# Kernel tuning notes

Measured on AMD Instinct MI355X. Metric: run time of the kernel, lower is better.

## Reference

```python
import jax, jax.numpy as jnp
import numpy as np

D_MODEL = 1024
N_HEAD = 16
HEAD_DIM = D_MODEL // N_HEAD
BATCH = 2
SEQ = 2048


def setup_inputs() -> dict:
    key = jax.random.key(0)
    ks = jax.random.split(key, 5)
    std = np.sqrt(2.0 / (D_MODEL + D_MODEL)).astype(np.float32)
    return {
        "in_features": jax.random.normal(ks[0], (BATCH, SEQ, D_MODEL), dtype=jnp.float32),
        "Wq": jax.random.normal(ks[1], (D_MODEL, D_MODEL), dtype=jnp.float32) * std,
        "Wk": jax.random.normal(ks[2], (D_MODEL, D_MODEL), dtype=jnp.float32) * std,
        "Wv": jax.random.normal(ks[3], (D_MODEL, D_MODEL), dtype=jnp.float32) * std,
        "Wo": jax.random.normal(ks[4], (D_MODEL, D_MODEL), dtype=jnp.float32) * std,
    }


def reference(in_features, Wq, Wk, Wv, Wo):
    B, S, _ = in_features.shape
    # projections: x @ W (custom Linear stores weight as [in, out], no bias)
    q = (in_features @ Wq).reshape(B, S, N_HEAD, HEAD_DIM).transpose(0, 2, 1, 3)  # [B,H,S,Dh]
    k = (in_features @ Wk).reshape(B, S, N_HEAD, HEAD_DIM).transpose(0, 2, 1, 3)
    v = (in_features @ Wv).reshape(B, S, N_HEAD, HEAD_DIM).transpose(0, 2, 1, 3)
    scale = HEAD_DIM ** (-0.5)
    scores = jnp.einsum("bhqd,bhkd->bhqk", q, k) * scale  # [B,H,S,S]
    causal = jnp.tril(jnp.ones((S, S), dtype=bool))
    scores = jnp.where(causal, scores, -jnp.inf)
    attn = jax.nn.softmax(scores, axis=-1)
    ctx = jnp.einsum("bhqk,bhkd->bhqd", attn, v)  # [B,H,S,Dh]
    ctx = ctx.transpose(0, 2, 1, 3).reshape(B, S, D_MODEL)
    return ctx @ Wo
```

## Files before the change

kernel.cpp:

```cpp
#include <hip/hip_runtime.h>
#include <hip/hip_bf16.h>

#define DM 1024
#define NH 16
#define HD 64
#define B_ 2
#define S_ 2048
#define M_ (B_*S_)

typedef __attribute__((ext_vector_type(8))) short bf16x8;
typedef __attribute__((ext_vector_type(4))) float f32x4;
typedef __attribute__((ext_vector_type(4))) unsigned uint32x4;
typedef __attribute__((ext_vector_type(2))) unsigned uint32x2;

__device__ __forceinline__ float bf2f(ushort u) {
  union { unsigned u32; float f; } c; c.u32 = ((unsigned)u) << 16; return c.f;
}
__device__ __forceinline__ ushort f2bf(float f) {
  union { float f; unsigned u32; } c; c.f = f;
  unsigned u = c.u32;
  unsigned r = (u + 0x7fffu + ((u >> 16) & 1u)) >> 16;
  return (ushort)r;
}
__device__ __forceinline__ unsigned fbits(float f) {
  union { float f; unsigned u; } c; c.f = f; return c.u;
}

__device__ __forceinline__ void async16(const ushort* g, ushort* l) {
  __builtin_amdgcn_global_load_lds((const __attribute__((address_space(1))) void*)g,
                                   (__attribute__((address_space(3))) void*)l, 16, 0, 0);
}

__device__ __forceinline__ void pswap32(unsigned& a, unsigned& b) {
  uint32x2 r = __builtin_amdgcn_permlane32_swap(a, b, false, false);
  a = r[0]; b = r[1];
}
__device__ __forceinline__ void pswap16(unsigned& a, unsigned& b) {
  uint32x2 r = __builtin_amdgcn_permlane16_swap(a, b, false, false);
  a = r[0]; b = r[1];
}

__global__ void cvt_prep(const float* __restrict__ x, const float* __restrict__ W0,
                         const float* __restrict__ W1, const float* __restrict__ W2,
                         const float* __restrict__ W3, ushort* __restrict__ wt,
                         ushort* __restrict__ xb) {
  __shared__ float tile[64][65];
  int z = blockIdx.z;
  int tx = threadIdx.x, ty = threadIdx.y;
  if (z == 4) {
    int tid = ty * 64 + tx;
    size_t base4 = ((size_t)blockIdx.y * 16 + blockIdx.x) * 4096;
    const float4* xv = (const float4*)x;
    ushort4* ov = (ushort4*)xb;
    #pragma unroll
    for (int k = 0; k < 16; ++k) {
      float4 v = xv[base4 + k * 256 + tid];
      ushort4 o;
      o.x = f2bf(v.x); o.y = f2bf(v.y); o.z = f2bf(v.z); o.w = f2bf(v.w);
      ov[base4 + k * 256 + tid] = o;
    }
    return;
  }
  const float* W = (z == 0) ? W0 : (z == 1) ? W1 : (z == 2) ? W2 : W3;
  ushort* Wt = wt + (size_t)z * (DM * DM);
  int c0 = blockIdx.x * 64, r0 = blockIdx.y * 64;
  #pragma unroll
  for (int i = ty; i < 64; i += 4) tile[i][tx] = W[(size_t)(r0 + i) * DM + c0 + tx];
  __syncthreads();
  #pragma unroll
  for (int i = ty; i < 64; i += 4) Wt[(size_t)(c0 + i) * DM + r0 + tx] = f2bf(tile[tx][i]);
}

template <int MODE, int BN>
__device__ __forceinline__ void gemm_body(const ushort* __restrict__ A,
                                          const ushort* __restrict__ Bt,
                                          ushort* __restrict__ Cb,
                                          float* __restrict__ Cf,
                                          ushort* As, ushort* Bs, ushort* Ts) {
  const int K = DM;
  constexpr int CN = BN / 32;
  int m0 = blockIdx.y * 128;
  int n0 = blockIdx.x * BN;
  int t = threadIdx.x;
  int lane = t & 63, wave = t >> 6;
  int wm = (wave >> 1) * 64, wn = (wave & 1) * (BN / 2);
  int lrow = lane & 15, quad = lane >> 4;

  int Ra = wave * 32;
  int Rb = wave * (BN / 4);
  int srow = lane >> 2, scol = (lane & 3) * 8;

  f32x4 acc[4][CN];
  #pragma unroll
  for (int r = 0; r < 4; ++r)
    #pragma unroll
    for (int c = 0; c < CN; ++c) acc[r][c] = (f32x4){0.f, 0.f, 0.f, 0.f};

  for (int k0 = 0; k0 < K; k0 += 32) {
    const ushort* ga = A + (size_t)(m0 + Ra + srow) * K + k0 + scol;
    const ushort* gb = Bt + (size_t)(n0 + Rb + srow) * K + k0 + scol;
    async16(ga,          As + Ra * 32);
    async16(ga + 16 * K, As + (Ra + 16) * 32);
    async16(gb,          Bs + Rb * 32);
    if (BN == 128) async16(gb + 16 * K, Bs + (Rb + 16) * 32);
    __syncthreads();

    bf16x8 af[4], bfr[CN];
    #pragma unroll
    for (int r = 0; r < 4; ++r)
      af[r] = *(const bf16x8*)(As + (wm + r * 16 + lrow) * 32 + quad * 8);
    #pragma unroll
    for (int c = 0; c < CN; ++c)
      bfr[c] = *(const bf16x8*)(Bs + (wn + c * 16 + lrow) * 32 + quad * 8);
    #pragma unroll
    for (int r = 0; r < 4; ++r)
      #pragma unroll
      for (int c = 0; c < CN; ++c)
        acc[r][c] = __builtin_amdgcn_mfma_f32_16x16x32_bf16(af[r], bfr[c], acc[r][c], 0, 0, 0);
    __syncthreads();
  }

  if constexpr (MODE == 2) {
    int bb = m0 >> 11;
    int s0base = m0 & 2047;
    #pragma unroll
    for (int H = 0; H < 2; ++H) {
      __syncthreads();
      if ((wave >> 1) == H) {
        #pragma unroll
        for (int r = 0; r < 4; ++r)
          #pragma unroll
          for (int c = 0; c < 4; ++c) {
            uint2 pk;
            pk.x = (unsigned)f2bf(acc[r][c][0]) | ((unsigned)f2bf(acc[r][c][1]) << 16);
            pk.y = (unsigned)f2bf(acc[r][c][2]) | ((unsigned)f2bf(acc[r][c][3]) << 16);
            *(uint2*)(Ts + (wn + c * 16 + lrow) * 72 + r * 16 + quad * 4) = pk;
          }
      }
      __syncthreads();
      #pragma unroll
      for (int i = 0; i < 4; ++i) {
        int id = t + i * 256;
        int nn = id >> 3, col = (id & 7) * 8;
        uint4 v = *(const uint4*)(Ts + nn * 72 + col);
        int h2 = (n0 >> 6) + (nn >> 6), d2 = nn & 63;
        size_t dst = (((size_t)(bb * NH + h2)) * HD + d2) * (size_t)S_ + s0base + H * 64 + col;
        *(uint4*)(Cb + dst) = v;
      }
    }
  } else {
    #pragma unroll
    for (int r = 0; r < 4; ++r) {
      #pragma unroll
      for (int c = 0; c < CN; ++c) {
        #pragma unroll
        for (int e = 0; e < 4; ++e) {
          int m = m0 + wm + r * 16 + quad * 4 + e;
          int n = n0 + wn + c * 16 + lrow;
          if (MODE == 0) {
            Cf[(size_t)m * DM + n] = acc[r][c][e];
          } else {
            int b = m >> 11, s = m & 2047, h = n >> 6, d = n & 63;
            Cb[(((size_t)(b * NH + h)) * S_ + s) * HD + d] = f2bf(acc[r][c][e]);
          }
        }
      }
    }
  }
}

__global__ __launch_bounds__(256, 3) void gemm_qkv(const ushort* __restrict__ A,
                                                   const ushort* __restrict__ wt,
                                                   ushort* __restrict__ qkv) {
  __shared__ __align__(16) ushort smem[9216];
  ushort* As = smem;
  ushort* Bs = smem + 4096;
  ushort* Ts = smem;
  int z = blockIdx.z;
  if (z < 2)
    gemm_body<1, 128>(A, wt + (size_t)z * (DM * DM), qkv + (size_t)z * ((size_t)M_ * DM),
                      nullptr, As, Bs, Ts);
  else
    gemm_body<2, 128>(A, wt + (size_t)2 * (DM * DM), qkv + (size_t)2 * ((size_t)M_ * DM),
                      nullptr, As, Bs, Ts);
}

__global__ __launch_bounds__(256, 3) void gemm_out(const ushort* __restrict__ A,
                                                   const ushort* __restrict__ wt,
                                                   float* __restrict__ C) {
  __shared__ __align__(16) ushort As[128 * 32];
  __shared__ __align__(16) ushort Bs[64 * 32];
  gemm_body<0, 64>(A, wt, nullptr, C, As, Bs, nullptr);
}

#define EXPC 0.18033688011f

struct AttnState {
  f32x4 o[4];
  float l;
};

template <bool MASKED>
__device__ __forceinline__ void attn_tile_compute(
    int q0, int kt, bf16x8 qf0, bf16x8 qf1,
    const bf16x8 kf0[4], const bf16x8 kf1[4],
    const bf16x8 vf0[4], const bf16x8 vf1[4],
    AttnState& st, int lrow, int quad) {
  f32x4 s[4];
  #pragma unroll
  for (int c = 0; c < 4; ++c) {
    f32x4 z = (f32x4){0.f, 0.f, 0.f, 0.f};
    z = __builtin_amdgcn_mfma_f32_16x16x32_bf16(kf0[c], qf0, z, 0, 0, 0);
    z = __builtin_amdgcn_mfma_f32_16x16x32_bf16(kf1[c], qf1, z, 0, 0, 0);
    s[c] = z;
  }
  int q = q0 + lrow;
  unsigned w0[4], w1[4];
  #pragma unroll
  for (int c = 0; c < 4; ++c) {
    float pv[4];
    #pragma unroll
    for (int e = 0; e < 4; ++e) {
      float v = __builtin_amdgcn_exp2f(s[c][e] * EXPC);
      if (MASKED) {
        int key = kt + c * 16 + quad * 4 + e;
        v = (key <= q) ? v : 0.f;
      }
      pv[e] = v;
      st.l += v;
    }
    w0[c] = __builtin_amdgcn_perm(fbits(pv[1]), fbits(pv[0]), 0x07060302u);
    w1[c] = __builtin_amdgcn_perm(fbits(pv[3]), fbits(pv[2]), 0x07060302u);
  }

  unsigned a0 = w0[0], b0 = w0[1]; pswap32(a0, b0); pswap16(a0, b0);
  unsigned a1 = w1[0], b1 = w1[1]; pswap32(a1, b1); pswap16(a1, b1);
  unsigned c0 = w0[2], d0 = w0[3]; pswap32(c0, d0); pswap16(c0, d0);
  unsigned c1 = w1[2], d1 = w1[3]; pswap32(c1, d1); pswap16(c1, d1);
  union { uint32x4 u; bf16x8 b; } P0, P1;
  P0.u = (uint32x4){a0, a1, b0, b1};
  P1.u = (uint32x4){c0, c1, d0, d1};

  #pragma unroll
  for (int dt = 0; dt < 4; ++dt) {
    st.o[dt] = __builtin_amdgcn_mfma_f32_16x16x32_bf16(P0.b, vf0[dt], st.o[dt], 0, 0, 0);
    st.o[dt] = __builtin_amdgcn_mfma_f32_16x16x32_bf16(P1.b, vf1[dt], st.o[dt], 0, 0, 0);
  }
}

__global__ __launch_bounds__(256, 2) void attn_mfma(const ushort* __restrict__ Q,
                                                    const ushort* __restrict__ Kmat,
                                                    const ushort* __restrict__ Vt,
                                                    ushort* __restrict__ ctx) {
  __shared__ __align__(16) ushort Ks[2][64 * 72];
  __shared__ __align__(16) ushort Vs[2][64 * 72];
  int t = threadIdx.x;
  int lane = t & 63, wave = t >> 6;
  int lrow = lane & 15, quad = lane >> 4;
  int n = blockIdx.x;
  int c = n & 255, g = n >> 8;
  int bh = c & 31;
  int j = (c >> 5) & 7;
  int qt = (g == 0) ? j : (g == 1) ? (15 - j) : (g == 2) ? (16 + j) : (31 - j);
  const ushort* Kb = Kmat + (size_t)bh * S_ * HD;
  const ushort* Vb = Vt + (size_t)bh * HD * S_;
  int b = bh >> 4, h = bh & 15;

  int r0 = t >> 3, s0 = (t & 7) * 8;
  int r1 = (t + 256) >> 3, s1 = s0;

  int q0 = qt * 64 + wave * 16;
  const ushort* Qp = Q + ((size_t)bh * S_ + q0) * HD;
  bf16x8 qf0 = *(const bf16x8*)(Qp + (size_t)lrow * HD + quad * 8);
  bf16x8 qf1 = *(const bf16x8*)(Qp + (size_t)lrow * HD + 32 + quad * 8);

  AttnState st;
  #pragma unroll
  for (int i = 0; i < 4; ++i) st.o[i] = (f32x4){0.f, 0.f, 0.f, 0.f};
  st.l = 0.f;

  int kend = qt * 64;

  {
    uint4 ka = *(const uint4*)(Kb + (size_t)r0 * HD + s0);
    uint4 kb2 = *(const uint4*)(Kb + (size_t)r1 * HD + s1);
    uint4 va = *(const uint4*)(Vb + (size_t)r0 * S_ + s0);
    uint4 vb2 = *(const uint4*)(Vb + (size_t)r1 * S_ + s1);
    *(uint4*)(Ks[0] + r0 * 72 + s0) = ka;
    *(uint4*)(Ks[0] + r1 * 72 + s1) = kb2;
    *(uint4*)(Vs[0] + r0 * 72 + s0) = va;
    *(uint4*)(Vs[0] + r1 * 72 + s1) = vb2;
  }
  __syncthreads();

  for (int kt = 0; kt <= kend; kt += 64) {
    int cur = (kt >> 6) & 1, nxt = cur ^ 1;
    bool has_next = (kt < kend);

    uint4 ka, kb2, va, vb2;
    if (has_next) {
      int ktn = kt + 64;
      ka  = *(const uint4*)(Kb + (size_t)(ktn + r0) * HD + s0);
      kb2 = *(const uint4*)(Kb + (size_t)(ktn + r1) * HD + s1);
      va  = *(const uint4*)(Vb + (size_t)r0 * S_ + ktn + s0);
      vb2 = *(const uint4*)(Vb + (size_t)r1 * S_ + ktn + s1);
    }

    bf16x8 kf0[4], kf1[4], vf0[4], vf1[4];
    #pragma unroll
    for (int c2 = 0; c2 < 4; ++c2) {
      const ushort* kr = Ks[cur] + (c2 * 16 + lrow) * 72;
      kf0[c2] = *(const bf16x8*)(kr + quad * 8);
      kf1[c2] = *(const bf16x8*)(kr + 32 + quad * 8);
      const ushort* vr = Vs[cur] + (c2 * 16 + lrow) * 72;
      vf0[c2] = *(const bf16x8*)(vr + quad * 8);
      vf1[c2] = *(const bf16x8*)(vr + 32 + quad * 8);
    }

    if (kt < kend)
      attn_tile_compute<false>(q0, kt, qf0, qf1, kf0, kf1, vf0, vf1, st, lrow, quad);
    else
      attn_tile_compute<true>(q0, kt, qf0, qf1, kf0, kf1, vf0, vf1, st, lrow, quad);

    if (has_next) {
      *(uint4*)(Ks[nxt] + r0 * 72 + s0) = ka;
      *(uint4*)(Ks[nxt] + r1 * 72 + s1) = kb2;
      *(uint4*)(Vs[nxt] + r0 * 72 + s0) = va;
      *(uint4*)(Vs[nxt] + r1 * 72 + s1) = vb2;
    }
    __syncthreads();
  }

  {
    float l = st.l;
    l += __shfl_xor(l, 16);
    l += __shfl_xor(l, 32);
    float rl = 1.0f / l;
    #pragma unroll
    for (int e = 0; e < 4; ++e) {
      float rinv = __shfl(rl, quad * 4 + e);
      int q = q0 + quad * 4 + e;
      #pragma unroll
      for (int dt = 0; dt < 4; ++dt)
        ctx[((size_t)b * S_ + q) * DM + h * HD + dt * 16 + lrow] = f2bf(st.o[dt][e] * rinv);
    }
  }
}

extern "C" void kernel_launch(void* const* d_in, const int* in_sizes, int n_in,
                              void* d_out, int out_size, void* d_ws, size_t ws_size,
                              hipStream_t stream) {
  const float* x  = (const float*)d_in[0];
  const float* Wq = (const float*)d_in[1];
  const float* Wk = (const float*)d_in[2];
  const float* Wv = (const float*)d_in[3];
  const float* Wo = (const float*)d_in[4];
  float* out = (float*)d_out;
  ushort* ws = (ushort*)d_ws;

  ushort* xb  = ws;
  ushort* wt  = xb + (size_t)M_ * DM;
  ushort* qkv = wt + (size_t)4 * DM * DM;
  ushort* ctx = qkv + (size_t)3 * M_ * DM;

  cvt_prep<<<dim3(16, 16, 5), dim3(64, 4), 0, stream>>>(x, Wq, Wk, Wv, Wo, wt, xb);
  gemm_qkv<<<dim3(DM / 128, M_ / 128, 3), 256, 0, stream>>>(xb, wt, qkv);
  attn_mfma<<<dim3(32 * B_ * NH), 256, 0, stream>>>(qkv, qkv + (size_t)M_ * DM,
                                                    qkv + (size_t)2 * M_ * DM, ctx);
  gemm_out<<<dim3(DM / 64, M_ / 128), 256, 0, stream>>>(ctx, wt + (size_t)3 * DM * DM, out);
}
```

Baseline: 177.0 us.

## Process two adjacent query tiles per attention block to reuse K/V tiles

Each attention block now handles 128 query rows, as two 64-row halves, instead of 64. Each K/V tile loaded into shared memory is applied to both halves, with the lower half stopping one tile earlier at its own diagonal. The grid shrinks from 1024 to 512 blocks, and the query-tile ordering is simplified to pair short and long blocks. This halves K/V global loads and LDS staging per query, but doubles per-thread register state, which may reduce occupancy. The smaller grid also risks leaving compute units underused on a large GPU.

```diff
diff --git a/kernel.cpp b/kernel.cpp
--- a/kernel.cpp
+++ b/kernel.cpp
@@ -261,7 +261,7 @@
   int c = n & 255, g = n >> 8;
   int bh = c & 31;
   int j = (c >> 5) & 7;
-  int qt = (g == 0) ? j : (g == 1) ? (15 - j) : (g == 2) ? (16 + j) : (31 - j);
+  int qt = g ? (15 - j) : j;
   const ushort* Kb = Kmat + (size_t)bh * S_ * HD;
   const ushort* Vb = Vt + (size_t)bh * HD * S_;
   int b = bh >> 4, h = bh & 15;
@@ -269,17 +269,25 @@
   int r0 = t >> 3, s0 = (t & 7) * 8;
   int r1 = (t + 256) >> 3, s1 = s0;
 
-  int q0 = qt * 64 + wave * 16;
-  const ushort* Qp = Q + ((size_t)bh * S_ + q0) * HD;
-  bf16x8 qf0 = *(const bf16x8*)(Qp + (size_t)lrow * HD + quad * 8);
-  bf16x8 qf1 = *(const bf16x8*)(Qp + (size_t)lrow * HD + 32 + quad * 8);
-
-  AttnState st;
-  #pragma unroll
-  for (int i = 0; i < 4; ++i) st.o[i] = (f32x4){0.f, 0.f, 0.f, 0.f};
-  st.l = 0.f;
-
-  int kend = qt * 64;
+  int q0L = qt * 128 + wave * 16;
+  int q0U = q0L + 64;
+  const ushort* QpL = Q + ((size_t)bh * S_ + q0L) * HD;
+  const ushort* QpU = Q + ((size_t)bh * S_ + q0U) * HD;
+  bf16x8 qL0 = *(const bf16x8*)(QpL + (size_t)lrow * HD + quad * 8);
+  bf16x8 qL1 = *(const bf16x8*)(QpL + (size_t)lrow * HD + 32 + quad * 8);
+  bf16x8 qU0 = *(const bf16x8*)(QpU + (size_t)lrow * HD + quad * 8);
+  bf16x8 qU1 = *(const bf16x8*)(QpU + (size_t)lrow * HD + 32 + quad * 8);
+
+  AttnState stL, stU;
+  #pragma unroll
+  for (int i = 0; i < 4; ++i) {
+    stL.o[i] = (f32x4){0.f, 0.f, 0.f, 0.f};
+    stU.o[i] = (f32x4){0.f, 0.f, 0.f, 0.f};
+  }
+  stL.l = 0.f; stU.l = 0.f;
+
+  int kend = (2 * qt + 1) * 64;
+  int kendL = kend - 64;
 
   {
     uint4 ka = *(const uint4*)(Kb + (size_t)r0 * HD + s0);
@@ -318,9 +326,13 @@
     }
 
     if (kt < kend)
-      attn_tile_compute<false>(q0, kt, qf0, qf1, kf0, kf1, vf0, vf1, st, lrow, quad);
+      attn_tile_compute<false>(q0U, kt, qU0, qU1, kf0, kf1, vf0, vf1, stU, lrow, quad);
     else
-      attn_tile_compute<true>(q0, kt, qf0, qf1, kf0, kf1, vf0, vf1, st, lrow, quad);
+      attn_tile_compute<true>(q0U, kt, qU0, qU1, kf0, kf1, vf0, vf1, stU, lrow, quad);
+    if (kt < kendL)
+      attn_tile_compute<false>(q0L, kt, qL0, qL1, kf0, kf1, vf0, vf1, stL, lrow, quad);
+    else if (kt == kendL)
+      attn_tile_compute<true>(q0L, kt, qL0, qL1, kf0, kf1, vf0, vf1, stL, lrow, quad);
 
     if (has_next) {
       *(uint4*)(Ks[nxt] + r0 * 72 + s0) = ka;
@@ -331,7 +343,10 @@
     __syncthreads();
   }
 
-  {
+  #pragma unroll
+  for (int half = 0; half < 2; ++half) {
+    AttnState& st = half ? stU : stL;
+    int q0 = half ? q0U : q0L;
     float l = st.l;
     l += __shfl_xor(l, 16);
     l += __shfl_xor(l, 32);
@@ -365,7 +380,7 @@
 
   cvt_prep<<<dim3(16, 16, 5), dim3(64, 4), 0, stream>>>(x, Wq, Wk, Wv, Wo, wt, xb);
   gemm_qkv<<<dim3(DM / 128, M_ / 128, 3), 256, 0, stream>>>(xb, wt, qkv);
-  attn_mfma<<<dim3(32 * B_ * NH), 256, 0, stream>>>(qkv, qkv + (size_t)M_ * DM,
+  attn_mfma<<<dim3(16 * B_ * NH), 256, 0, stream>>>(qkv, qkv + (size_t)M_ * DM,
                                                     qkv + (size_t)2 * M_ * DM, ctx);
   gemm_out<<<dim3(DM / 64, M_ / 128), 256, 0, stream>>>(ctx, wt + (size_t)3 * DM * DM, out);
 }
```

New measurement: 182.3 us. 3.0% more time.

## Load K/V fragments directly from global memory, dropping LDS staging and barriers

Applied to the files above, without the earlier changes.

The attention kernel no longer stages K and V tiles through double-buffered shared memory. Each wave now loads its MFMA fragments straight from global memory, which removes the LDS writes, the LDS reads and the per-iteration __syncthreads. The cost is that each of the four waves fetches the same K/V data separately, so the kernel leans on L1/L2 for reuse. The software prefetch of the next tile is also gone, so global load latency is no longer overlapped with compute.

```diff
diff --git a/kernel.cpp b/kernel.cpp
--- a/kernel.cpp
+++ b/kernel.cpp
@@ -252,8 +252,6 @@
                                                     const ushort* __restrict__ Kmat,
                                                     const ushort* __restrict__ Vt,
                                                     ushort* __restrict__ ctx) {
-  __shared__ __align__(16) ushort Ks[2][64 * 72];
-  __shared__ __align__(16) ushort Vs[2][64 * 72];
   int t = threadIdx.x;
   int lane = t & 63, wave = t >> 6;
   int lrow = lane & 15, quad = lane >> 4;
@@ -266,9 +264,6 @@
   const ushort* Vb = Vt + (size_t)bh * HD * S_;
   int b = bh >> 4, h = bh & 15;
 
-  int r0 = t >> 3, s0 = (t & 7) * 8;
-  int r1 = (t + 256) >> 3, s1 = s0;
-
   int q0 = qt * 64 + wave * 16;
   const ushort* Qp = Q + ((size_t)bh * S_ + q0) * HD;
   bf16x8 qf0 = *(const bf16x8*)(Qp + (size_t)lrow * HD + quad * 8);
@@ -281,54 +276,26 @@
 
   int kend = qt * 64;
 
-  {
-    uint4 ka = *(const uint4*)(Kb + (size_t)r0 * HD + s0);
-    uint4 kb2 = *(const uint4*)(Kb + (size_t)r1 * HD + s1);
-    uint4 va = *(const uint4*)(Vb + (size_t)r0 * S_ + s0);
-    uint4 vb2 = *(const uint4*)(Vb + (size_t)r1 * S_ + s1);
-    *(uint4*)(Ks[0] + r0 * 72 + s0) = ka;
-    *(uint4*)(Ks[0] + r1 * 72 + s1) = kb2;
-    *(uint4*)(Vs[0] + r0 * 72 + s0) = va;
-    *(uint4*)(Vs[0] + r1 * 72 + s1) = vb2;
-  }
-  __syncthreads();
-
+  int kq = quad * 8;
   for (int kt = 0; kt <= kend; kt += 64) {
-    int cur = (kt >> 6) & 1, nxt = cur ^ 1;
-    bool has_next = (kt < kend);
-
-    uint4 ka, kb2, va, vb2;
-    if (has_next) {
-      int ktn = kt + 64;
-      ka  = *(const uint4*)(Kb + (size_t)(ktn + r0) * HD + s0);
-      kb2 = *(const uint4*)(Kb + (size_t)(ktn + r1) * HD + s1);
-      va  = *(const uint4*)(Vb + (size_t)r0 * S_ + ktn + s0);
-      vb2 = *(const uint4*)(Vb + (size_t)r1 * S_ + ktn + s1);
-    }
+    const ushort* Kp = Kb + (size_t)kt * HD;
+    const ushort* Vp = Vb + kt;
 
     bf16x8 kf0[4], kf1[4], vf0[4], vf1[4];
     #pragma unroll
     for (int c2 = 0; c2 < 4; ++c2) {
-      const ushort* kr = Ks[cur] + (c2 * 16 + lrow) * 72;
-      kf0[c2] = *(const bf16x8*)(kr + quad * 8);
-      kf1[c2] = *(const bf16x8*)(kr + 32 + quad * 8);
-      const ushort* vr = Vs[cur] + (c2 * 16 + lrow) * 72;
-      vf0[c2] = *(const bf16x8*)(vr + quad * 8);
-      vf1[c2] = *(const bf16x8*)(vr + 32 + quad * 8);
+      const ushort* kr = Kp + (size_t)(c2 * 16 + lrow) * HD + kq;
+      kf0[c2] = *(const bf16x8*)(kr);
+      kf1[c2] = *(const bf16x8*)(kr + 32);
+      const ushort* vr = Vp + (size_t)(c2 * 16 + lrow) * S_ + kq;
+      vf0[c2] = *(const bf16x8*)(vr);
+      vf1[c2] = *(const bf16x8*)(vr + 32);
     }
 
     if (kt < kend)
       attn_tile_compute<false>(q0, kt, qf0, qf1, kf0, kf1, vf0, vf1, st, lrow, quad);
     else
       attn_tile_compute<true>(q0, kt, qf0, qf1, kf0, kf1, vf0, vf1, st, lrow, quad);
-
-    if (has_next) {
-      *(uint4*)(Ks[nxt] + r0 * 72 + s0) = ka;
-      *(uint4*)(Ks[nxt] + r1 * 72 + s1) = kb2;
-      *(uint4*)(Vs[nxt] + r0 * 72 + s0) = va;
-      *(uint4*)(Vs[nxt] + r1 * 72 + s1) = vb2;
-    }
-    __syncthreads();
   }
 
   {
```

New measurement: 255.9 us. +44.6%, slower.
